# Kernel tuning notes

Measured on AMD Instinct MI355X. Metric: run time of the kernel, lower is better.

Reference implementation:

```python
import jax, jax.numpy as jnp
import numpy as np

EPS_F = 1e-6   # epsilon_F global in original repo
GAMMA = 0.8
K = 5
BN_EPS = 1e-5
M = 128
N = 100000
E = 1600000
MY = 10

def setup_inputs() -> dict:
    key = jax.random.key(0)
    ks = jax.random.split(key, 6)
    X = jax.random.normal(ks[0], (M, N), dtype=jnp.float32)
    # xavier_uniform for F: limit = sqrt(6/(m+m))
    lim = float(np.sqrt(6.0 / (M + M)))
    F_mat = jax.random.uniform(ks[1], (M, M), dtype=jnp.float32, minval=-lim, maxval=lim)
    B = (1.0 / np.sqrt(M)) * jax.random.normal(ks[2], (MY, M), dtype=jnp.float32)
    bn_weight = jnp.ones((M,), dtype=jnp.float32)
    bn_bias = jnp.zeros((M,), dtype=jnp.float32)
    edge_val = jax.random.uniform(ks[3], (E,), dtype=jnp.float32)
    edge_row = jax.random.randint(ks[4], (E,), 0, N, dtype=jnp.int64 if jax.config.jax_enable_x64 else jnp.int32)
    edge_col = jax.random.randint(ks[5], (E,), 0, N, dtype=jnp.int64 if jax.config.jax_enable_x64 else jnp.int32)
    return {"X": X, "F_mat": F_mat, "B": B, "bn_weight": bn_weight,
            "bn_bias": bn_bias, "edge_val": edge_val,
            "edge_row": edge_row, "edge_col": edge_col}

def reference(X, F_mat, B, bn_weight, bn_bias, edge_val, edge_row, edge_col):
    n = X.shape[1]
    # normalized Gram matrix g(F) = F^T F / (||F^T F||_fro + eps)
    FF = F_mat.T @ F_mat                       # [m, m]
    G = FF / (jnp.linalg.norm(FF) + EPS_F)
    X_first = X                                # [m, n]

    def step(Xc, _):
        Y = Xc.T                               # [n, m]
        # SpMM: (S_t @ Y)[r] += val * Y[c]
        SY = jax.ops.segment_sum(edge_val[:, None] * Y[edge_col], edge_row,
                                 num_segments=n)   # [n, m]
        Xn = GAMMA * (G @ SY.T) + X_first          # [m, n]
        return Xn, None

    Xk, _ = jax.lax.scan(step, X, None, length=K)
    out = Xk.T                                 # [n, m]
    # BatchNorm1d over feature dim (training-mode batch stats); dropout omitted (eval)
    mu = out.mean(axis=0)
    var = out.var(axis=0)
    out = (out - mu) * jax.lax.rsqrt(var + BN_EPS) * bn_weight + bn_bias
    return out @ B.T                           # [n, m_y]
```

## Files before the change

### kernel.cpp

```cpp
#include <hip/hip_runtime.h>
#include <math.h>

#define MDIM 128
#define MY 10
#define GAMMA 0.8f
#define KITER 5

__device__ __forceinline__ float bf2f(unsigned short h) {
    return __uint_as_float(((unsigned int)h) << 16);
}
__device__ __forceinline__ unsigned short f2bf(float f) {
    unsigned int u = __float_as_uint(f);
    u += 0x7fffu + ((u >> 16) & 1u);
    return (unsigned short)(u >> 16);
}

__global__ void k_transpose(const float* __restrict__ X, float* __restrict__ Y0,
                            unsigned short* __restrict__ Y0h, int n) {
    __shared__ float tile[32][33];
    int r0 = blockIdx.x * 32;
    int f0 = blockIdx.y * 32;
    int tx = threadIdx.x, ty = threadIdx.y;
    #pragma unroll
    for (int i = 0; i < 32; i += 8) {
        tile[ty + i][tx] = X[(size_t)(f0 + ty + i) * n + (r0 + tx)];
    }
    __syncthreads();
    #pragma unroll
    for (int i = 0; i < 32; i += 8) {
        float v = tile[tx][ty + i];
        Y0[(size_t)(r0 + ty + i) * MDIM + (f0 + tx)] = v;
        Y0h[(size_t)(r0 + ty + i) * MDIM + (f0 + tx)] = f2bf(v);
    }
}

__global__ void k_gram(const float* __restrict__ F, float* __restrict__ FF,
                       float* __restrict__ normAcc) {
    int i = blockIdx.x, j = threadIdx.x;
    float acc = 0.f;
    for (int k = 0; k < MDIM; ++k)
        acc = fmaf(F[k * MDIM + i], F[k * MDIM + j], acc);
    FF[i * MDIM + j] = acc;
    __shared__ float red[MDIM];
    red[j] = acc * acc;
    __syncthreads();
    for (int s = 64; s > 0; s >>= 1) {
        if (j < s) red[j] += red[j + s];
        __syncthreads();
    }
    if (j == 0) atomicAdd(normAcc, red[0]);
}

__global__ void k_gnorm(const float* __restrict__ FF, const float* __restrict__ normAcc,
                        float* __restrict__ G) {
    int idx = blockIdx.x * 256 + threadIdx.x;
    float s = GAMMA / (sqrtf(*normAcc) + 1e-6f);
    G[idx] = FF[idx] * s;
}

__global__ void k_hist(const int* __restrict__ erow, int* __restrict__ cnt, int E) {
    int e = blockIdx.x * 256 + threadIdx.x;
    if (e < E) atomicAdd(&cnt[erow[e]], 1);
}

__global__ void k_scan1(const int* __restrict__ cnt, int* __restrict__ blockSums, int n) {
    int tid = threadIdx.x;
    int base = blockIdx.x * 1024 + tid * 4;
    int s = 0;
    if (base + 3 < n) {
        int4 v = *(const int4*)&cnt[base];
        s = v.x + v.y + v.z + v.w;
    } else {
        for (int i = 0; i < 4; ++i)
            if (base + i < n) s += cnt[base + i];
    }
    __shared__ int red[256];
    red[tid] = s;
    __syncthreads();
    for (int st = 128; st > 0; st >>= 1) {
        if (tid < st) red[tid] += red[tid + st];
        __syncthreads();
    }
    if (tid == 0) blockSums[blockIdx.x] = red[0];
}

__global__ void k_scan2(int* __restrict__ blockSums, int* __restrict__ row_off,
                        int nb, int n) {
    __shared__ int s[256];
    int tid = threadIdx.x;
    int v = (tid < nb) ? blockSums[tid] : 0;
    s[tid] = v;
    __syncthreads();
    for (int off = 1; off < 256; off <<= 1) {
        int t = (tid >= off) ? s[tid - off] : 0;
        __syncthreads();
        s[tid] += t;
        __syncthreads();
    }
    if (tid < nb) blockSums[tid] = s[tid] - v;
    if (tid == 0) row_off[n] = s[255];
}

__global__ void k_scan3(const int* __restrict__ cnt, const int* __restrict__ blockOff,
                        int* __restrict__ row_off, int n) {
    int tid = threadIdx.x;
    int base = blockIdx.x * 1024 + tid * 4;
    int v[4];
    #pragma unroll
    for (int i = 0; i < 4; ++i) v[i] = (base + i < n) ? cnt[base + i] : 0;
    int local = v[0] + v[1] + v[2] + v[3];
    __shared__ int s[256];
    s[tid] = local;
    __syncthreads();
    for (int off = 1; off < 256; off <<= 1) {
        int t = (tid >= off) ? s[tid - off] : 0;
        __syncthreads();
        s[tid] += t;
        __syncthreads();
    }
    int excl = s[tid] - local + blockOff[blockIdx.x];
    #pragma unroll
    for (int i = 0; i < 4; ++i) {
        if (base + i < n) { row_off[base + i] = excl; excl += v[i]; }
    }
}

__global__ void k_scatter(const int* __restrict__ erow, const int* __restrict__ ecol,
                          const float* __restrict__ eval_, int* __restrict__ cursor,
                          int* __restrict__ csr_col, float* __restrict__ csr_val, int E) {
    int e = blockIdx.x * 256 + threadIdx.x;
    if (e < E) {
        int r = erow[e];
        int pos = atomicAdd(&cursor[r], 1);
        csr_col[pos] = ecol[e];
        csr_val[pos] = eval_[e];
    }
}

__global__ void __launch_bounds__(256) k_spmm(const unsigned short* __restrict__ Yh,
                                              const int* __restrict__ row_off,
                                              const int* __restrict__ csr_col,
                                              const float* __restrict__ csr_val,
                                              float* __restrict__ SY, int n) {
    int row = blockIdx.x * 8 + (threadIdx.x >> 5);
    int tx = threadIdx.x & 31;
    if (row >= n) return;
    int e0 = row_off[row], e1 = row_off[row + 1];
    float4 acc = make_float4(0.f, 0.f, 0.f, 0.f);
    int e = e0;
    for (; e + 4 <= e1; e += 4) {
        float v0 = csr_val[e + 0];
        float v1 = csr_val[e + 1];
        float v2 = csr_val[e + 2];
        float v3 = csr_val[e + 3];
        int c0 = csr_col[e + 0];
        int c1 = csr_col[e + 1];
        int c2 = csr_col[e + 2];
        int c3 = csr_col[e + 3];
        ushort4 h0 = *(const ushort4*)&Yh[(size_t)c0 * MDIM + tx * 4];
        ushort4 h1 = *(const ushort4*)&Yh[(size_t)c1 * MDIM + tx * 4];
        ushort4 h2 = *(const ushort4*)&Yh[(size_t)c2 * MDIM + tx * 4];
        ushort4 h3 = *(const ushort4*)&Yh[(size_t)c3 * MDIM + tx * 4];
        acc.x = fmaf(v0, bf2f(h0.x), acc.x);
        acc.y = fmaf(v0, bf2f(h0.y), acc.y);
        acc.z = fmaf(v0, bf2f(h0.z), acc.z);
        acc.w = fmaf(v0, bf2f(h0.w), acc.w);
        acc.x = fmaf(v1, bf2f(h1.x), acc.x);
        acc.y = fmaf(v1, bf2f(h1.y), acc.y);
        acc.z = fmaf(v1, bf2f(h1.z), acc.z);
        acc.w = fmaf(v1, bf2f(h1.w), acc.w);
        acc.x = fmaf(v2, bf2f(h2.x), acc.x);
        acc.y = fmaf(v2, bf2f(h2.y), acc.y);
        acc.z = fmaf(v2, bf2f(h2.z), acc.z);
        acc.w = fmaf(v2, bf2f(h2.w), acc.w);
        acc.x = fmaf(v3, bf2f(h3.x), acc.x);
        acc.y = fmaf(v3, bf2f(h3.y), acc.y);
        acc.z = fmaf(v3, bf2f(h3.z), acc.z);
        acc.w = fmaf(v3, bf2f(h3.w), acc.w);
    }
    for (; e < e1; ++e) {
        float v = csr_val[e];
        int c = csr_col[e];
        ushort4 h = *(const ushort4*)&Yh[(size_t)c * MDIM + tx * 4];
        acc.x = fmaf(v, bf2f(h.x), acc.x);
        acc.y = fmaf(v, bf2f(h.y), acc.y);
        acc.z = fmaf(v, bf2f(h.z), acc.z);
        acc.w = fmaf(v, bf2f(h.w), acc.w);
    }
    *(float4*)&SY[(size_t)row * MDIM + tx * 4] = acc;
}

__global__ void __launch_bounds__(256) k_gemm(const float* __restrict__ SY,
                                              const float* __restrict__ G,
                                              const float* __restrict__ Y0,
                                              float* __restrict__ Yout,
                                              unsigned short* __restrict__ Yhout,
                                              int writeH, int n) {
    __shared__ float sG[MDIM * MDIM];
    int tid = threadIdx.x;
    #pragma unroll
    for (int i = 0; i < 16; ++i) {
        int idx = (i * 256 + tid) * 4;
        *(float4*)&sG[idx] = *(const float4*)&G[idx];
    }
    __syncthreads();
    int tx = tid & 31, ty = tid >> 5;
    size_t r0 = (size_t)blockIdx.x * 32 + ty * 4;
    int f0 = tx * 4;
    float4 acc[4];
    #pragma unroll
    for (int i = 0; i < 4; ++i) acc[i] = make_float4(0.f, 0.f, 0.f, 0.f);
    for (int j = 0; j < MDIM; j += 4) {
        float4 g0 = *(const float4*)&sG[(j + 0) * MDIM + f0];
        float4 g1 = *(const float4*)&sG[(j + 1) * MDIM + f0];
        float4 g2 = *(const float4*)&sG[(j + 2) * MDIM + f0];
        float4 g3 = *(const float4*)&sG[(j + 3) * MDIM + f0];
        #pragma unroll
        for (int i = 0; i < 4; ++i) {
            float4 sr = *(const float4*)&SY[(r0 + i) * MDIM + j];
            acc[i].x = fmaf(sr.x, g0.x, acc[i].x);
            acc[i].y = fmaf(sr.x, g0.y, acc[i].y);
            acc[i].z = fmaf(sr.x, g0.z, acc[i].z);
            acc[i].w = fmaf(sr.x, g0.w, acc[i].w);
            acc[i].x = fmaf(sr.y, g1.x, acc[i].x);
            acc[i].y = fmaf(sr.y, g1.y, acc[i].y);
            acc[i].z = fmaf(sr.y, g1.z, acc[i].z);
            acc[i].w = fmaf(sr.y, g1.w, acc[i].w);
            acc[i].x = fmaf(sr.z, g2.x, acc[i].x);
            acc[i].y = fmaf(sr.z, g2.y, acc[i].y);
            acc[i].z = fmaf(sr.z, g2.z, acc[i].z);
            acc[i].w = fmaf(sr.z, g2.w, acc[i].w);
            acc[i].x = fmaf(sr.w, g3.x, acc[i].x);
            acc[i].y = fmaf(sr.w, g3.y, acc[i].y);
            acc[i].z = fmaf(sr.w, g3.z, acc[i].z);
            acc[i].w = fmaf(sr.w, g3.w, acc[i].w);
        }
    }
    #pragma unroll
    for (int i = 0; i < 4; ++i) {
        float4 y0 = *(const float4*)&Y0[(r0 + i) * MDIM + f0];
        float4 o;
        o.x = acc[i].x + y0.x;
        o.y = acc[i].y + y0.y;
        o.z = acc[i].z + y0.z;
        o.w = acc[i].w + y0.w;
        *(float4*)&Yout[(r0 + i) * MDIM + f0] = o;
        if (writeH) {
            ushort4 h;
            h.x = f2bf(o.x);
            h.y = f2bf(o.y);
            h.z = f2bf(o.z);
            h.w = f2bf(o.w);
            *(ushort4*)&Yhout[(r0 + i) * MDIM + f0] = h;
        }
    }
}

__global__ void k_bnstats(const float* __restrict__ Y, float* __restrict__ stats, int n) {
    int f = threadIdx.x;
    int chunk = (n + gridDim.x - 1) / gridDim.x;
    int rbeg = blockIdx.x * chunk;
    int rend = rbeg + chunk;
    if (rend > n) rend = n;
    float s = 0.f, sq = 0.f;
    for (int r = rbeg; r < rend; ++r) {
        float v = Y[(size_t)r * MDIM + f];
        s += v;
        sq = fmaf(v, v, sq);
    }
    atomicAdd(&stats[f], s);
    atomicAdd(&stats[MDIM + f], sq);
}

__global__ void k_finalize(const float* __restrict__ stats, const float* __restrict__ B,
                           const float* __restrict__ bnw, const float* __restrict__ bnb,
                           float* __restrict__ Bs, float* __restrict__ cvec, int n) {
    int f = threadIdx.x;
    float inv_n = 1.f / (float)n;
    float mu = stats[f] * inv_n;
    float var = stats[MDIM + f] * inv_n - mu * mu;
    float rs = rsqrtf(var + 1e-5f);
    float sw = rs * bnw[f];
    float cv = bnb[f] - mu * sw;
    __shared__ float red[MDIM];
    for (int o = 0; o < MY; ++o) {
        float b = B[o * MDIM + f];
        Bs[o * MDIM + f] = b * sw;
        red[f] = b * cv;
        __syncthreads();
        for (int s = 64; s > 0; s >>= 1) {
            if (f < s) red[f] += red[f + s];
            __syncthreads();
        }
        if (f == 0) cvec[o] = red[0];
        __syncthreads();
    }
}

__global__ void __launch_bounds__(256) k_project(const float* __restrict__ Y,
                                                 const float* __restrict__ Bs,
                                                 const float* __restrict__ cvec,
                                                 float* __restrict__ out, int n) {
    __shared__ float yt[16 * 129];
    __shared__ float sB[MY * 129];
    __shared__ float sc[MY];
    int tid = threadIdx.x;
    size_t rbase = (size_t)blockIdx.x * 16;
    for (int idx = tid; idx < 16 * MDIM; idx += 256) {
        int r = idx >> 7, f = idx & 127;
        yt[r * 129 + f] = Y[(rbase + r) * MDIM + f];
    }
    for (int idx = tid; idx < MY * MDIM; idx += 256) {
        int o = idx >> 7, f = idx & 127;
        sB[o * 129 + f] = Bs[idx];
    }
    if (tid < MY) sc[tid] = cvec[tid];
    __syncthreads();
    if (tid < 16 * MY) {
        int r = tid / MY, o = tid % MY;
        float acc = sc[o];
        for (int f = 0; f < MDIM; ++f)
            acc = fmaf(yt[r * 129 + f], sB[o * 129 + f], acc);
        out[(rbase + r) * MY + o] = acc;
    }
}

extern "C" void kernel_launch(void* const* d_in, const int* in_sizes, int n_in,
                              void* d_out, int out_size, void* d_ws, size_t ws_size,
                              hipStream_t stream) {
    const float* X    = (const float*)d_in[0];
    const float* F    = (const float*)d_in[1];
    const float* B    = (const float*)d_in[2];
    const float* bnw  = (const float*)d_in[3];
    const float* bnb  = (const float*)d_in[4];
    const float* ev   = (const float*)d_in[5];
    const int*   erow = (const int*)d_in[6];
    const int*   ecol = (const int*)d_in[7];
    float* out = (float*)d_out;
    const int n = in_sizes[0] / MDIM;
    const int E = in_sizes[5];

    char* w = (char*)d_ws;
    size_t off = 0;
    auto carve = [&](size_t bytes) -> void* {
        void* p = w + off;
        off += (bytes + 255) & ~(size_t)255;
        return p;
    };
    float*          Y0    = (float*)carve((size_t)n * MDIM * 4);
    float*          Ycur  = (float*)carve((size_t)n * MDIM * 4);
    float*          SY    = (float*)carve((size_t)n * MDIM * 4);
    unsigned short* Yh    = (unsigned short*)carve((size_t)n * MDIM * 2);
    float* FF        = (float*)carve(MDIM * MDIM * 4);
    float* G         = (float*)carve(MDIM * MDIM * 4);
    float* csr_val   = (float*)carve((size_t)E * 4);
    int*   csr_col   = (int*)carve((size_t)E * 4);
    int*   row_off   = (int*)carve((size_t)(n + 1) * 4);
    int*   cursor    = (int*)carve((size_t)n * 4);
    int*   cnt       = (int*)carve((size_t)n * 4);
    int*   blockSums = (int*)carve(1024 * 4);
    float* normAcc   = (float*)carve(4);
    float* stats     = (float*)carve(2 * MDIM * 4);
    float* Bs        = (float*)carve(MY * MDIM * 4);
    float* cvec      = (float*)carve(MY * 4);
    (void)ws_size;

    hipMemsetAsync(cnt, 0, (size_t)n * 4, stream);
    hipMemsetAsync(normAcc, 0, 4, stream);
    hipMemsetAsync(stats, 0, 2 * MDIM * 4, stream);

    k_transpose<<<dim3(n / 32, MDIM / 32), dim3(32, 8), 0, stream>>>(X, Y0, Yh, n);
    k_gram<<<MDIM, MDIM, 0, stream>>>(F, FF, normAcc);
    k_gnorm<<<MDIM * MDIM / 256, 256, 0, stream>>>(FF, normAcc, G);

    const int nb = (n + 1023) / 1024;
    k_hist<<<(E + 255) / 256, 256, 0, stream>>>(erow, cnt, E);
    k_scan1<<<nb, 256, 0, stream>>>(cnt, blockSums, n);
    k_scan2<<<1, 256, 0, stream>>>(blockSums, row_off, nb, n);
    k_scan3<<<nb, 256, 0, stream>>>(cnt, blockSums, row_off, n);
    hipMemcpyAsync(cursor, row_off, (size_t)n * 4, hipMemcpyDeviceToDevice, stream);
    k_scatter<<<(E + 255) / 256, 256, 0, stream>>>(erow, ecol, ev, cursor, csr_col, csr_val, E);

    for (int k = 0; k < KITER; ++k) {
        k_spmm<<<(n + 7) / 8, 256, 0, stream>>>(Yh, row_off, csr_col, csr_val, SY, n);
        int writeH = (k < KITER - 1) ? 1 : 0;
        k_gemm<<<n / 32, 256, 0, stream>>>(SY, G, Y0, Ycur, Yh, writeH, n);
    }

    k_bnstats<<<256, MDIM, 0, stream>>>(Ycur, stats, n);
    k_finalize<<<1, MDIM, 0, stream>>>(stats, B, bnw, bnb, Bs, cvec, n);
    k_project<<<n / 16, 256, 0, stream>>>(Ycur, Bs, cvec, out, n);
}
```

Baseline: 1.117 ms.

## Interleave CSR col/val records, fuse cursor init into scan, add nontemporal accesses

Packs the CSR column index and value into one 8-byte record so each edge needs a single load in the SpMM instead of two separate array loads. It writes the cursor copy directly from the scan kernel, dropping a device-to-device memcpy. It also marks streaming loads and stores of SY, Y0, Ycur and the edge records as nontemporal to keep cache space for the randomly gathered Yh rows. The risk is that nontemporal hints on SY, which is written and then immediately re-read by the GEMM, could raise traffic if the data would otherwise have stayed in cache.

```diff
diff --git a/kernel.cpp b/kernel.cpp
--- a/kernel.cpp
+++ b/kernel.cpp
@@ -5,6 +5,9 @@
 #define MY 10
 #define GAMMA 0.8f
 #define KITER 5
+
+typedef float v4f __attribute__((ext_vector_type(4)));
+typedef int   v2i __attribute__((ext_vector_type(2)));
 
 __device__ __forceinline__ float bf2f(unsigned short h) {
     return __uint_as_float(((unsigned int)h) << 16);
@@ -102,7 +105,7 @@
 }
 
 __global__ void k_scan3(const int* __restrict__ cnt, const int* __restrict__ blockOff,
-                        int* __restrict__ row_off, int n) {
+                        int* __restrict__ row_off, int* __restrict__ cursor, int n) {
     int tid = threadIdx.x;
     int base = blockIdx.x * 1024 + tid * 4;
     int v[4];
@@ -121,26 +124,31 @@
     int excl = s[tid] - local + blockOff[blockIdx.x];
     #pragma unroll
     for (int i = 0; i < 4; ++i) {
-        if (base + i < n) { row_off[base + i] = excl; excl += v[i]; }
+        if (base + i < n) {
+            row_off[base + i] = excl;
+            cursor[base + i] = excl;
+            excl += v[i];
+        }
     }
 }
 
 __global__ void k_scatter(const int* __restrict__ erow, const int* __restrict__ ecol,
                           const float* __restrict__ eval_, int* __restrict__ cursor,
-                          int* __restrict__ csr_col, float* __restrict__ csr_val, int E) {
+                          v2i* __restrict__ rec, int E) {
     int e = blockIdx.x * 256 + threadIdx.x;
     if (e < E) {
         int r = erow[e];
         int pos = atomicAdd(&cursor[r], 1);
-        csr_col[pos] = ecol[e];
-        csr_val[pos] = eval_[e];
+        v2i rv;
+        rv.x = ecol[e];
+        rv.y = __float_as_int(eval_[e]);
+        __builtin_nontemporal_store(rv, &rec[pos]);
     }
 }
 
 __global__ void __launch_bounds__(256) k_spmm(const unsigned short* __restrict__ Yh,
                                               const int* __restrict__ row_off,
-                                              const int* __restrict__ csr_col,
-                                              const float* __restrict__ csr_val,
+                                              const v2i* __restrict__ rec,
                                               float* __restrict__ SY, int n) {
     int row = blockIdx.x * 8 + (threadIdx.x >> 5);
     int tx = threadIdx.x & 31;
@@ -149,18 +157,18 @@
     float4 acc = make_float4(0.f, 0.f, 0.f, 0.f);
     int e = e0;
     for (; e + 4 <= e1; e += 4) {
-        float v0 = csr_val[e + 0];
-        float v1 = csr_val[e + 1];
-        float v2 = csr_val[e + 2];
-        float v3 = csr_val[e + 3];
-        int c0 = csr_col[e + 0];
-        int c1 = csr_col[e + 1];
-        int c2 = csr_col[e + 2];
-        int c3 = csr_col[e + 3];
-        ushort4 h0 = *(const ushort4*)&Yh[(size_t)c0 * MDIM + tx * 4];
-        ushort4 h1 = *(const ushort4*)&Yh[(size_t)c1 * MDIM + tx * 4];
-        ushort4 h2 = *(const ushort4*)&Yh[(size_t)c2 * MDIM + tx * 4];
-        ushort4 h3 = *(const ushort4*)&Yh[(size_t)c3 * MDIM + tx * 4];
+        v2i r0_ = __builtin_nontemporal_load(&rec[e + 0]);
+        v2i r1_ = __builtin_nontemporal_load(&rec[e + 1]);
+        v2i r2_ = __builtin_nontemporal_load(&rec[e + 2]);
+        v2i r3_ = __builtin_nontemporal_load(&rec[e + 3]);
+        ushort4 h0 = *(const ushort4*)&Yh[(size_t)r0_.x * MDIM + tx * 4];
+        ushort4 h1 = *(const ushort4*)&Yh[(size_t)r1_.x * MDIM + tx * 4];
+        ushort4 h2 = *(const ushort4*)&Yh[(size_t)r2_.x * MDIM + tx * 4];
+        ushort4 h3 = *(const ushort4*)&Yh[(size_t)r3_.x * MDIM + tx * 4];
+        float v0 = __int_as_float(r0_.y);
+        float v1 = __int_as_float(r1_.y);
+        float v2 = __int_as_float(r2_.y);
+        float v3 = __int_as_float(r3_.y);
         acc.x = fmaf(v0, bf2f(h0.x), acc.x);
         acc.y = fmaf(v0, bf2f(h0.y), acc.y);
         acc.z = fmaf(v0, bf2f(h0.z), acc.z);
@@ -179,15 +187,17 @@
         acc.w = fmaf(v3, bf2f(h3.w), acc.w);
     }
     for (; e < e1; ++e) {
-        float v = csr_val[e];
-        int c = csr_col[e];
-        ushort4 h = *(const ushort4*)&Yh[(size_t)c * MDIM + tx * 4];
+        v2i r0_ = __builtin_nontemporal_load(&rec[e]);
+        float v = __int_as_float(r0_.y);
+        ushort4 h = *(const ushort4*)&Yh[(size_t)r0_.x * MDIM + tx * 4];
         acc.x = fmaf(v, bf2f(h.x), acc.x);
         acc.y = fmaf(v, bf2f(h.y), acc.y);
         acc.z = fmaf(v, bf2f(h.z), acc.z);
         acc.w = fmaf(v, bf2f(h.w), acc.w);
     }
-    *(float4*)&SY[(size_t)row * MDIM + tx * 4] = acc;
+    v4f o;
+    o.x = acc.x; o.y = acc.y; o.z = acc.z; o.w = acc.w;
+    __builtin_nontemporal_store(o, (v4f*)&SY[(size_t)row * MDIM + tx * 4]);
 }
 
 __global__ void __launch_bounds__(256) k_gemm(const float* __restrict__ SY,
@@ -217,7 +227,9 @@
         float4 g3 = *(const float4*)&sG[(j + 3) * MDIM + f0];
         #pragma unroll
         for (int i = 0; i < 4; ++i) {
-            float4 sr = *(const float4*)&SY[(r0 + i) * MDIM + j];
+            v4f srv = __builtin_nontemporal_load((const v4f*)&SY[(r0 + i) * MDIM + j]);
+            float4 sr;
+            sr.x = srv.x; sr.y = srv.y; sr.z = srv.z; sr.w = srv.w;
             acc[i].x = fmaf(sr.x, g0.x, acc[i].x);
             acc[i].y = fmaf(sr.x, g0.y, acc[i].y);
             acc[i].z = fmaf(sr.x, g0.z, acc[i].z);
@@ -238,13 +250,13 @@
     }
     #pragma unroll
     for (int i = 0; i < 4; ++i) {
-        float4 y0 = *(const float4*)&Y0[(r0 + i) * MDIM + f0];
-        float4 o;
+        v4f y0 = __builtin_nontemporal_load((const v4f*)&Y0[(r0 + i) * MDIM + f0]);
+        v4f o;
         o.x = acc[i].x + y0.x;
         o.y = acc[i].y + y0.y;
         o.z = acc[i].z + y0.z;
         o.w = acc[i].w + y0.w;
-        *(float4*)&Yout[(r0 + i) * MDIM + f0] = o;
+        __builtin_nontemporal_store(o, (v4f*)&Yout[(r0 + i) * MDIM + f0]);
         if (writeH) {
             ushort4 h;
             h.x = f2bf(o.x);
@@ -353,8 +365,7 @@
     unsigned short* Yh    = (unsigned short*)carve((size_t)n * MDIM * 2);
     float* FF        = (float*)carve(MDIM * MDIM * 4);
     float* G         = (float*)carve(MDIM * MDIM * 4);
-    float* csr_val   = (float*)carve((size_t)E * 4);
-    int*   csr_col   = (int*)carve((size_t)E * 4);
+    v2i*   rec       = (v2i*)carve((size_t)E * 8);
     int*   row_off   = (int*)carve((size_t)(n + 1) * 4);
     int*   cursor    = (int*)carve((size_t)n * 4);
     int*   cnt       = (int*)carve((size_t)n * 4);
@@ -377,12 +388,11 @@
     k_hist<<<(E + 255) / 256, 256, 0, stream>>>(erow, cnt, E);
     k_scan1<<<nb, 256, 0, stream>>>(cnt, blockSums, n);
     k_scan2<<<1, 256, 0, stream>>>(blockSums, row_off, nb, n);
-    k_scan3<<<nb, 256, 0, stream>>>(cnt, blockSums, row_off, n);
-    hipMemcpyAsync(cursor, row_off, (size_t)n * 4, hipMemcpyDeviceToDevice, stream);
-    k_scatter<<<(E + 255) / 256, 256, 0, stream>>>(erow, ecol, ev, cursor, csr_col, csr_val, E);
+    k_scan3<<<nb, 256, 0, stream>>>(cnt, blockSums, row_off, cursor, n);
+    k_scatter<<<(E + 255) / 256, 256, 0, stream>>>(erow, ecol, ev, cursor, rec, E);
 
     for (int k = 0; k < KITER; ++k) {
-        k_spmm<<<(n + 7) / 8, 256, 0, stream>>>(Yh, row_off, csr_col, csr_val, SY, n);
+        k_spmm<<<(n + 7) / 8, 256, 0, stream>>>(Yh, row_off, rec, SY, n);
         int writeH = (k < KITER - 1) ? 1 : 0;
         k_gemm<<<n / 32, 256, 0, stream>>>(SY, G, Y0, Ycur, Yh, writeH, n);
     }
```

Result: slower. 1.403 ms (+25.5%).
